# Performance work log

Hardware: AMD Instinct MI355X
Metric: run time of the kernel (lower is better)

Reference implementation:

```python
import jax, jax.numpy as jnp
import numpy as np

EMB_DIM = 768
HEAD_SIZE = 64


def setup_inputs() -> dict:
    key = jax.random.key(0)
    kx, kk, kq, kv = jax.random.split(key, 4)
    B, S = 8, 2048
    bound = 1.0 / np.sqrt(EMB_DIM)  # torch Linear default init range
    x = jax.random.normal(kx, (B, S, EMB_DIM), dtype=jnp.float32)
    Wk = jax.random.uniform(kk, (EMB_DIM, HEAD_SIZE), jnp.float32, -bound, bound)
    Wq = jax.random.uniform(kq, (EMB_DIM, HEAD_SIZE), jnp.float32, -bound, bound)
    Wv = jax.random.uniform(kv, (EMB_DIM, HEAD_SIZE), jnp.float32, -bound, bound)
    return {"x": x, "Wk": Wk, "Wq": Wq, "Wv": Wv}


def reference(x, Wk, Wq, Wv):
    # bias-free projections: [b, s, d] @ [d, h] -> [b, s, h]
    key = jnp.einsum("bsd,dh->bsh", x, Wk)
    query = jnp.einsum("bsd,dh->bsh", x, Wq)
    value = jnp.einsum("bsd,dh->bsh", x, Wv)
    scale = 1.0 / jnp.sqrt(jnp.asarray(HEAD_SIZE, dtype=x.dtype))
    # [b, q, k] attention scores
    scores = jnp.einsum("bqh,bkh->bqk", query, key) * scale
    probs = jax.nn.softmax(scores, axis=-1)
    # weighted value sum: [b, q, h]
    out = jnp.einsum("bqk,bkh->bqh", probs, value)
    return out
```

## Files before the change

### kernel.cpp

```cpp
#include <hip/hip_runtime.h>
#include <hip/hip_bf16.h>
#include <stdint.h>

#define B_ 8
#define S_ 2048
#define D_ 768
#define H_ 64
#define M_ (B_*S_)

typedef __attribute__((ext_vector_type(8))) short bf16x8;
typedef __attribute__((ext_vector_type(4))) float f32x4;
typedef __attribute__((ext_vector_type(4))) float floatv4;
typedef __attribute__((ext_vector_type(4))) unsigned short u16x4;
typedef __attribute__((ext_vector_type(8))) unsigned short u16x8;

__device__ __forceinline__ uint16_t f2bf(float f) {
    union { float f; uint32_t u; } c; c.f = f;
    return (uint16_t)((c.u + 0x7FFFu + ((c.u >> 16) & 1u)) >> 16);
}

__device__ __forceinline__ void load_lds16(const void* g, void* l) {
    __builtin_amdgcn_global_load_lds(
        (const __attribute__((address_space(1))) uint32_t*)(const uint32_t*)g,
        (__attribute__((address_space(3))) uint32_t*)(uint32_t*)l,
        16, 0, 0);
}

__global__ __launch_bounds__(256) void k_convert_w(const float* __restrict__ Wk,
                                                   const float* __restrict__ Wq,
                                                   const float* __restrict__ Wv,
                                                   uint16_t* __restrict__ wt) {
    const int mat = blockIdx.y;
    const float* W = mat == 0 ? Wk : (mat == 1 ? Wq : Wv);
    const float scale = (mat == 1) ? 0.18033688011f : 1.0f;
    uint16_t* out = wt + (size_t)mat * (H_ * D_);
    int i = blockIdx.x * 256 + threadIdx.x;
    int d = i >> 6, h = i & 63;
    out[h * D_ + d] = f2bf(W[i] * scale);
}

__global__ __launch_bounds__(512, 2) void k_proj(const float* __restrict__ x,
                                                 const uint16_t* __restrict__ wt,
                                                 uint16_t* __restrict__ kb,
                                                 uint16_t* __restrict__ qb,
                                                 uint16_t* __restrict__ vt) {
    __shared__ char lds[65536];
    const int tid  = threadIdx.x;
    const int lane = tid & 63, wave = tid >> 6;
    const int l15  = lane & 15, g = lane >> 4;
    const int m0   = blockIdx.x * 64;
    const int mrow = (wave >> 1) * 16;
    const int nb   = (wave & 1) * 32;

    const int trow = tid >> 3, tc8 = tid & 7;
    const float* xrowp = x + (size_t)(m0 + trow) * D_ + tc8 * 8;
    const int xw = trow * 128 + ((tc8 ^ (trow & 7)) << 4);

    const int cswz = (((lane & 7) ^ (lane >> 3)) << 4);
    const char* wsrc[3];
    int wdst[3];
#pragma unroll
    for (int j = 0; j < 3; ++j) {
        int c = wave * 3 + j, mat = c >> 3, wrow = (c & 7) * 8 + (lane >> 3);
        wsrc[j] = (const char*)(wt + (size_t)mat * (H_ * D_) + (size_t)wrow * D_) + cswz;
        wdst[j] = 16384 + c * 1024;
    }

    floatv4 xr[12][2];
#pragma unroll
    for (int kt = 0; kt < 12; ++kt) {
        xr[kt][0] = *(const floatv4*)(xrowp + kt * 64);
        xr[kt][1] = *(const floatv4*)(xrowp + kt * 64 + 4);
    }

#pragma unroll
    for (int j = 0; j < 3; ++j)
        load_lds16(wsrc[j], lds + wdst[j]);
    {
        u16x8 cv;
        cv[0]=f2bf(xr[0][0][0]); cv[1]=f2bf(xr[0][0][1]); cv[2]=f2bf(xr[0][0][2]); cv[3]=f2bf(xr[0][0][3]);
        cv[4]=f2bf(xr[0][1][0]); cv[5]=f2bf(xr[0][1][1]); cv[6]=f2bf(xr[0][1][2]); cv[7]=f2bf(xr[0][1][3]);
        *(u16x8*)(lds + xw) = cv;
    }
    __syncthreads();

    f32x4 acc[3][2] = {};

#pragma unroll
    for (int kt = 0; kt < 12; ++kt) {
        const int cur = kt & 1, nxt = cur ^ 1;
        if (kt < 11) {
#pragma unroll
            for (int j = 0; j < 3; ++j)
                load_lds16(wsrc[j] + (size_t)(kt + 1) * 128, lds + nxt * 24576 + wdst[j]);
        }
        const char* xsb = lds + cur * 8192;
        const char* wsb = lds + 16384 + cur * 24576;
        bf16x8 a[2], b[3][2][2];
#pragma unroll
        for (int kk = 0; kk < 2; ++kk) {
            int row = mrow + l15;
            a[kk] = *(const bf16x8*)(xsb + row * 128 + ((kk*64 + g*16) ^ ((row & 7) << 4)));
        }
#pragma unroll
        for (int mat = 0; mat < 3; ++mat)
#pragma unroll
            for (int n = 0; n < 2; ++n)
#pragma unroll
                for (int kk = 0; kk < 2; ++kk) {
                    int row = nb + n * 16 + l15;
                    b[mat][n][kk] = *(const bf16x8*)(wsb + mat * 8192 + row * 128 +
                                                     ((kk*64 + g*16) ^ ((row & 7) << 4)));
                }
#pragma unroll
        for (int mat = 0; mat < 3; ++mat)
#pragma unroll
            for (int n = 0; n < 2; ++n)
#pragma unroll
                for (int kk = 0; kk < 2; ++kk)
                    acc[mat][n] = __builtin_amdgcn_mfma_f32_16x16x32_bf16(
                                      a[kk], b[mat][n][kk], acc[mat][n], 0, 0, 0);
        if (kt < 11) {
            u16x8 cv;
            cv[0]=f2bf(xr[kt+1][0][0]); cv[1]=f2bf(xr[kt+1][0][1]);
            cv[2]=f2bf(xr[kt+1][0][2]); cv[3]=f2bf(xr[kt+1][0][3]);
            cv[4]=f2bf(xr[kt+1][1][0]); cv[5]=f2bf(xr[kt+1][1][1]);
            cv[6]=f2bf(xr[kt+1][1][2]); cv[7]=f2bf(xr[kt+1][1][3]);
            *(u16x8*)(lds + nxt * 8192 + xw) = cv;
        }
        __syncthreads();
    }

#pragma unroll
    for (int mat = 0; mat < 3; ++mat)
#pragma unroll
        for (int n = 0; n < 2; ++n) {
            int col  = nb + n * 16 + l15;
            int row0 = m0 + mrow + g * 4;
            if (mat < 2) {
                uint16_t* out = (mat == 0) ? kb : qb;
#pragma unroll
                for (int r = 0; r < 4; ++r)
                    out[(size_t)(row0 + r) * H_ + col] = f2bf(acc[mat][n][r]);
            } else {
                int bb = row0 >> 11, s = row0 & 2047;
                u16x4 pk;
#pragma unroll
                for (int r = 0; r < 4; ++r) pk[r] = f2bf(acc[mat][n][r]);
                *(u16x4*)(vt + ((size_t)bb * H_ + col) * S_ + s) = pk;
            }
        }
}

__global__ __launch_bounds__(256) void k_attn(const uint16_t* __restrict__ qb,
                                              const uint16_t* __restrict__ kb,
                                              const uint16_t* __restrict__ vt,
                                              float* __restrict__ out) {
    __shared__ char plds[4][4096];
    __shared__ float o_buf[4 * 32 * 64];
    __shared__ float l_buf[4][32];
    const int tid  = threadIdx.x;
    const int lane = tid & 63, wave = tid >> 6;
    const int l15 = lane & 15, g = lane >> 4;
    const int batch = blockIdx.y;
    const int q0 = blockIdx.x * 32;
    const size_t qrow = (size_t)batch * S_ + q0;
    const float MBIAS = 4.0f;

    bf16x8 aq[2][2];
#pragma unroll
    for (int qm = 0; qm < 2; ++qm)
#pragma unroll
        for (int kk = 0; kk < 2; ++kk)
            aq[qm][kk] = *(const bf16x8*)(qb + (qrow + qm*16 + l15) * H_ + kk*32 + g*8);

    f32x4 o[2][4] = {};
    float Ls[2][4] = {};

    const uint16_t* kbase = kb + (size_t)batch * S_ * H_;
    const uint16_t* vbase = vt + (size_t)batch * H_ * S_;
    char* pl = plds[wave];
    const int kt0 = wave * 8;

    bf16x8 bk[4][2], bkn[4][2];
#pragma unroll
    for (int n = 0; n < 4; ++n)
#pragma unroll
        for (int kk = 0; kk < 2; ++kk)
            bk[n][kk] = *(const bf16x8*)(kbase + (size_t)(kt0*64 + n*16 + l15) * H_ + kk*32 + g*8);

#pragma unroll
    for (int j = 0; j < 8; ++j) {
        const int kt = kt0 + j;
        if (j < 7) {
#pragma unroll
            for (int n = 0; n < 4; ++n)
#pragma unroll
                for (int kk = 0; kk < 2; ++kk)
                    bkn[n][kk] = *(const bf16x8*)(kbase + (size_t)((kt+1)*64 + n*16 + l15) * H_ + kk*32 + g*8);
        }
        f32x4 s[2][4] = {};
#pragma unroll
        for (int qm = 0; qm < 2; ++qm)
#pragma unroll
            for (int n = 0; n < 4; ++n)
#pragma unroll
                for (int kk = 0; kk < 2; ++kk)
                    s[qm][n] = __builtin_amdgcn_mfma_f32_16x16x32_bf16(
                                   aq[qm][kk], bk[n][kk], s[qm][n], 0, 0, 0);

        bf16x8 bv[4][2];
#pragma unroll
        for (int nh = 0; nh < 4; ++nh)
#pragma unroll
            for (int kk = 0; kk < 2; ++kk)
                bv[nh][kk] = *(const bf16x8*)(vbase + (size_t)(nh*16 + l15) * S_ + kt*64 + kk*32 + g*8);

#pragma unroll
        for (int qm = 0; qm < 2; ++qm)
#pragma unroll
            for (int r = 0; r < 4; ++r) {
                int row = qm*16 + g*4 + r;
#pragma unroll
                for (int n = 0; n < 4; ++n) {
                    float p = exp2f(s[qm][n][r] - MBIAS);
                    Ls[qm][r] += p;
                    int cb  = ((n*16 + l15) * 2) ^ ((row & 7) << 4);
                    *(uint16_t*)(pl + row*128 + cb) = f2bf(p);
                }
            }

        bf16x8 pa[2][2];
#pragma unroll
        for (int qm = 0; qm < 2; ++qm)
#pragma unroll
            for (int kk = 0; kk < 2; ++kk) {
                int row = qm*16 + l15;
                int cb  = (kk*64 + g*16) ^ ((row & 7) << 4);
                pa[qm][kk] = *(const bf16x8*)(pl + row*128 + cb);
            }
#pragma unroll
        for (int qm = 0; qm < 2; ++qm)
#pragma unroll
            for (int nh = 0; nh < 4; ++nh)
#pragma unroll
                for (int kk = 0; kk < 2; ++kk)
                    o[qm][nh] = __builtin_amdgcn_mfma_f32_16x16x32_bf16(
                                    pa[qm][kk], bv[nh][kk], o[qm][nh], 0, 0, 0);
        if (j < 7) {
#pragma unroll
            for (int n = 0; n < 4; ++n)
#pragma unroll
                for (int kk = 0; kk < 2; ++kk)
                    bk[n][kk] = bkn[n][kk];
        }
    }

#pragma unroll
    for (int qm = 0; qm < 2; ++qm)
#pragma unroll
        for (int r = 0; r < 4; ++r) {
            float l = Ls[qm][r];
#pragma unroll
            for (int off = 1; off < 16; off <<= 1) l += __shfl_xor(l, off);
            Ls[qm][r] = l;
        }
    if (l15 == 0) {
#pragma unroll
        for (int qm = 0; qm < 2; ++qm)
#pragma unroll
            for (int r = 0; r < 4; ++r)
                l_buf[wave][qm*16 + g*4 + r] = Ls[qm][r];
    }
#pragma unroll
    for (int qm = 0; qm < 2; ++qm)
#pragma unroll
        for (int nh = 0; nh < 4; ++nh)
#pragma unroll
            for (int r = 0; r < 4; ++r) {
                int i = qm*16 + nh*4 + r;
                o_buf[(wave*32 + i)*64 + lane] = o[qm][nh][r];
            }
    __syncthreads();

    const int iw0 = wave * 8;
    const int qm0 = iw0 >> 4;
    float rinv[4];
#pragma unroll
    for (int r = 0; r < 4; ++r) {
        int row = qm0*16 + g*4 + r;
        rinv[r] = 1.0f / (l_buf[0][row] + l_buf[1][row] + l_buf[2][row] + l_buf[3][row]);
    }
    float* obase = out + qrow * H_;
#pragma unroll
    for (int ii = 0; ii < 8; ++ii) {
        int i = iw0 + ii;
        int nh = (i >> 2) & 3, r = i & 3;
        float tot = o_buf[(0*32 + i)*64 + lane] + o_buf[(1*32 + i)*64 + lane]
                  + o_buf[(2*32 + i)*64 + lane] + o_buf[(3*32 + i)*64 + lane];
        int row = qm0*16 + g*4 + r, col = nh*16 + l15;
        obase[(size_t)row * H_ + col] = tot * rinv[r];
    }
}

extern "C" void kernel_launch(void* const* d_in, const int* in_sizes, int n_in,
                              void* d_out, int out_size, void* d_ws, size_t ws_size,
                              hipStream_t stream) {
    const float* x  = (const float*)d_in[0];
    const float* Wk = (const float*)d_in[1];
    const float* Wq = (const float*)d_in[2];
    const float* Wv = (const float*)d_in[3];
    float* out = (float*)d_out;

    uint16_t* ws = (uint16_t*)d_ws;
    uint16_t* wt = ws;
    uint16_t* kb = wt + (size_t)3 * H_ * D_;
    uint16_t* qb = kb + (size_t)M_ * H_;
    uint16_t* vt = qb + (size_t)M_ * H_;

    k_convert_w<<<dim3(192, 3), dim3(256), 0, stream>>>(Wk, Wq, Wv, wt);
    k_proj<<<dim3(M_ / 64), dim3(512), 0, stream>>>(x, wt, kb, qb, vt);
    k_attn<<<dim3(S_ / 32, B_), dim3(256), 0, stream>>>(qb, kb, vt, out);
}
```

Baseline: 130.8 us.

## Halve projection tile rows and interleave two key tiles per attention iteration

The projection kernel now processes 32 rows per block instead of 64, with each wave computing one 16-column slice across the three matrices. This doubles the grid and cuts per-thread register and LDS use, at the cost of reloading the weights more often. The attention kernel now handles two independent key tiles per loop iteration with separate score, probability buffer and output accumulators, exposing more independent MFMA and memory work to hide latency. The cost is more register pressure and the loss of explicit next-tile K prefetch.

```diff
diff --git a/kernel.cpp b/kernel.cpp
--- a/kernel.cpp
+++ b/kernel.cpp
@@ -39,22 +39,22 @@
     out[h * D_ + d] = f2bf(W[i] * scale);
 }
 
-__global__ __launch_bounds__(512, 2) void k_proj(const float* __restrict__ x,
-                                                 const uint16_t* __restrict__ wt,
-                                                 uint16_t* __restrict__ kb,
-                                                 uint16_t* __restrict__ qb,
-                                                 uint16_t* __restrict__ vt) {
-    __shared__ char lds[65536];
+__global__ __launch_bounds__(512) void k_proj(const float* __restrict__ x,
+                                              const uint16_t* __restrict__ wt,
+                                              uint16_t* __restrict__ kb,
+                                              uint16_t* __restrict__ qb,
+                                              uint16_t* __restrict__ vt) {
+    __shared__ char lds[57344];
     const int tid  = threadIdx.x;
     const int lane = tid & 63, wave = tid >> 6;
     const int l15  = lane & 15, g = lane >> 4;
-    const int m0   = blockIdx.x * 64;
-    const int mrow = (wave >> 1) * 16;
-    const int nb   = (wave & 1) * 32;
-
-    const int trow = tid >> 3, tc8 = tid & 7;
-    const float* xrowp = x + (size_t)(m0 + trow) * D_ + tc8 * 8;
-    const int xw = trow * 128 + ((tc8 ^ (trow & 7)) << 4);
+    const int m0   = blockIdx.x * 32;
+    const int mrow = (wave & 1) * 16;
+    const int nc   = (wave >> 1) * 16;
+
+    const int trow = tid >> 4, tc = tid & 15;
+    const float* xrowp = x + (size_t)(m0 + trow) * D_ + tc * 4;
+    const int xw = trow * 128 + (((tc >> 1) ^ (trow & 7)) << 4) + (tc & 1) * 8;
 
     const int cswz = (((lane & 7) ^ (lane >> 3)) << 4);
     const char* wsrc[3];
@@ -63,28 +63,25 @@
     for (int j = 0; j < 3; ++j) {
         int c = wave * 3 + j, mat = c >> 3, wrow = (c & 7) * 8 + (lane >> 3);
         wsrc[j] = (const char*)(wt + (size_t)mat * (H_ * D_) + (size_t)wrow * D_) + cswz;
-        wdst[j] = 16384 + c * 1024;
-    }
-
-    floatv4 xr[12][2];
-#pragma unroll
-    for (int kt = 0; kt < 12; ++kt) {
-        xr[kt][0] = *(const floatv4*)(xrowp + kt * 64);
-        xr[kt][1] = *(const floatv4*)(xrowp + kt * 64 + 4);
-    }
+        wdst[j] = 8192 + c * 1024;
+    }
+
+    floatv4 xr[12];
+#pragma unroll
+    for (int kt = 0; kt < 12; ++kt)
+        xr[kt] = *(const floatv4*)(xrowp + kt * 64);
 
 #pragma unroll
     for (int j = 0; j < 3; ++j)
         load_lds16(wsrc[j], lds + wdst[j]);
     {
-        u16x8 cv;
-        cv[0]=f2bf(xr[0][0][0]); cv[1]=f2bf(xr[0][0][1]); cv[2]=f2bf(xr[0][0][2]); cv[3]=f2bf(xr[0][0][3]);
-        cv[4]=f2bf(xr[0][1][0]); cv[5]=f2bf(xr[0][1][1]); cv[6]=f2bf(xr[0][1][2]); cv[7]=f2bf(xr[0][1][3]);
-        *(u16x8*)(lds + xw) = cv;
+        u16x4 cv;
+        cv[0]=f2bf(xr[0][0]); cv[1]=f2bf(xr[0][1]); cv[2]=f2bf(xr[0][2]); cv[3]=f2bf(xr[0][3]);
+        *(u16x4*)(lds + xw) = cv;
     }
     __syncthreads();
 
-    f32x4 acc[3][2] = {};
+    f32x4 acc[3] = {};
 
 #pragma unroll
     for (int kt = 0; kt < 12; ++kt) {
@@ -94,9 +91,9 @@
             for (int j = 0; j < 3; ++j)
                 load_lds16(wsrc[j] + (size_t)(kt + 1) * 128, lds + nxt * 24576 + wdst[j]);
         }
-        const char* xsb = lds + cur * 8192;
-        const char* wsb = lds + 16384 + cur * 24576;
-        bf16x8 a[2], b[3][2][2];
+        const char* xsb = lds + cur * 4096;
+        const char* wsb = lds + 8192 + cur * 24576;
+        bf16x8 a[2], b[3][2];
 #pragma unroll
         for (int kk = 0; kk < 2; ++kk) {
             int row = mrow + l15;
@@ -105,60 +102,50 @@
 #pragma unroll
         for (int mat = 0; mat < 3; ++mat)
 #pragma unroll
-            for (int n = 0; n < 2; ++n)
-#pragma unroll
-                for (int kk = 0; kk < 2; ++kk) {
-                    int row = nb + n * 16 + l15;
-                    b[mat][n][kk] = *(const bf16x8*)(wsb + mat * 8192 + row * 128 +
-                                                     ((kk*64 + g*16) ^ ((row & 7) << 4)));
-                }
+            for (int kk = 0; kk < 2; ++kk) {
+                int row = nc + l15;
+                b[mat][kk] = *(const bf16x8*)(wsb + mat * 8192 + row * 128 +
+                                              ((kk*64 + g*16) ^ ((row & 7) << 4)));
+            }
 #pragma unroll
         for (int mat = 0; mat < 3; ++mat)
 #pragma unroll
-            for (int n = 0; n < 2; ++n)
-#pragma unroll
-                for (int kk = 0; kk < 2; ++kk)
-                    acc[mat][n] = __builtin_amdgcn_mfma_f32_16x16x32_bf16(
-                                      a[kk], b[mat][n][kk], acc[mat][n], 0, 0, 0);
+            for (int kk = 0; kk < 2; ++kk)
+                acc[mat] = __builtin_amdgcn_mfma_f32_16x16x32_bf16(
+                               a[kk], b[mat][kk], acc[mat], 0, 0, 0);
         if (kt < 11) {
-            u16x8 cv;
-            cv[0]=f2bf(xr[kt+1][0][0]); cv[1]=f2bf(xr[kt+1][0][1]);
-            cv[2]=f2bf(xr[kt+1][0][2]); cv[3]=f2bf(xr[kt+1][0][3]);
-            cv[4]=f2bf(xr[kt+1][1][0]); cv[5]=f2bf(xr[kt+1][1][1]);
-            cv[6]=f2bf(xr[kt+1][1][2]); cv[7]=f2bf(xr[kt+1][1][3]);
-            *(u16x8*)(lds + nxt * 8192 + xw) = cv;
+            u16x4 cv;
+            cv[0]=f2bf(xr[kt+1][0]); cv[1]=f2bf(xr[kt+1][1]);
+            cv[2]=f2bf(xr[kt+1][2]); cv[3]=f2bf(xr[kt+1][3]);
+            *(u16x4*)(lds + nxt * 4096 + xw) = cv;
         }
         __syncthreads();
     }
 
 #pragma unroll
-    for (int mat = 0; mat < 3; ++mat)
-#pragma unroll
-        for (int n = 0; n < 2; ++n) {
-            int col  = nb + n * 16 + l15;
-            int row0 = m0 + mrow + g * 4;
-            if (mat < 2) {
-                uint16_t* out = (mat == 0) ? kb : qb;
-#pragma unroll
-                for (int r = 0; r < 4; ++r)
-                    out[(size_t)(row0 + r) * H_ + col] = f2bf(acc[mat][n][r]);
-            } else {
-                int bb = row0 >> 11, s = row0 & 2047;
-                u16x4 pk;
-#pragma unroll
-                for (int r = 0; r < 4; ++r) pk[r] = f2bf(acc[mat][n][r]);
-                *(u16x4*)(vt + ((size_t)bb * H_ + col) * S_ + s) = pk;
-            }
-        }
+    for (int mat = 0; mat < 3; ++mat) {
+        int col  = nc + l15;
+        int row0 = m0 + mrow + g * 4;
+        if (mat < 2) {
+            uint16_t* out = (mat == 0) ? kb : qb;
+#pragma unroll
+            for (int r = 0; r < 4; ++r)
+                out[(size_t)(row0 + r) * H_ + col] = f2bf(acc[mat][r]);
+        } else {
+            int bb = row0 >> 11, s = row0 & 2047;
+            u16x4 pk;
+#pragma unroll
+            for (int r = 0; r < 4; ++r) pk[r] = f2bf(acc[mat][r]);
+            *(u16x4*)(vt + ((size_t)bb * H_ + col) * S_ + s) = pk;
+        }
+    }
 }
 
 __global__ __launch_bounds__(256) void k_attn(const uint16_t* __restrict__ qb,
                                               const uint16_t* __restrict__ kb,
                                               const uint16_t* __restrict__ vt,
                                               float* __restrict__ out) {
-    __shared__ char plds[4][4096];
-    __shared__ float o_buf[4 * 32 * 64];
-    __shared__ float l_buf[4][32];
+    __shared__ char smem[65536];
     const int tid  = threadIdx.x;
     const int lane = tid & 63, wave = tid >> 6;
     const int l15 = lane & 15, g = lane >> 4;
@@ -167,6 +154,8 @@
     const size_t qrow = (size_t)batch * S_ + q0;
     const float MBIAS = 4.0f;
 
+    float* o_buf = (float*)(smem + 32768);
+
     bf16x8 aq[2][2];
 #pragma unroll
     for (int qm = 0; qm < 2; ++qm)
@@ -174,47 +163,66 @@
         for (int kk = 0; kk < 2; ++kk)
             aq[qm][kk] = *(const bf16x8*)(qb + (qrow + qm*16 + l15) * H_ + kk*32 + g*8);
 
-    f32x4 o[2][4] = {};
-    float Ls[2][4] = {};
+    f32x4 o[2][2][4] = {};
+    float Ls[2][2][4] = {};
 
     const uint16_t* kbase = kb + (size_t)batch * S_ * H_;
     const uint16_t* vbase = vt + (size_t)batch * H_ * S_;
-    char* pl = plds[wave];
+    char* pl0 = smem + wave * 8192;
+    char* pl1 = pl0 + 4096;
     const int kt0 = wave * 8;
 
-    bf16x8 bk[4][2], bkn[4][2];
-#pragma unroll
-    for (int n = 0; n < 4; ++n)
-#pragma unroll
-        for (int kk = 0; kk < 2; ++kk)
-            bk[n][kk] = *(const bf16x8*)(kbase + (size_t)(kt0*64 + n*16 + l15) * H_ + kk*32 + g*8);
-
-#pragma unroll
-    for (int j = 0; j < 8; ++j) {
-        const int kt = kt0 + j;
-        if (j < 7) {
+#pragma unroll
+    for (int i = 0; i < 4; ++i) {
+        const int ktA = kt0 + i, ktB = kt0 + 4 + i;
+
+        f32x4 sA[2][4] = {};
+        bf16x8 bvA[4][2];
+        {
+            bf16x8 bk[4][2];
 #pragma unroll
             for (int n = 0; n < 4; ++n)
 #pragma unroll
                 for (int kk = 0; kk < 2; ++kk)
-                    bkn[n][kk] = *(const bf16x8*)(kbase + (size_t)((kt+1)*64 + n*16 + l15) * H_ + kk*32 + g*8);
-        }
-        f32x4 s[2][4] = {};
-#pragma unroll
-        for (int qm = 0; qm < 2; ++qm)
+                    bk[n][kk] = *(const bf16x8*)(kbase + (size_t)(ktA*64 + n*16 + l15) * H_ + kk*32 + g*8);
+#pragma unroll
+            for (int qm = 0; qm < 2; ++qm)
+#pragma unroll
+                for (int n = 0; n < 4; ++n)
+#pragma unroll
+                    for (int kk = 0; kk < 2; ++kk)
+                        sA[qm][n] = __builtin_amdgcn_mfma_f32_16x16x32_bf16(
+                                        aq[qm][kk], bk[n][kk], sA[qm][n], 0, 0, 0);
+#pragma unroll
+            for (int nh = 0; nh < 4; ++nh)
+#pragma unroll
+                for (int kk = 0; kk < 2; ++kk)
+                    bvA[nh][kk] = *(const bf16x8*)(vbase + (size_t)(nh*16 + l15) * S_ + ktA*64 + kk*32 + g*8);
+        }
+
+        f32x4 sB[2][4] = {};
+        bf16x8 bvB[4][2];
+        {
+            bf16x8 bk[4][2];
 #pragma unroll
             for (int n = 0; n < 4; ++n)
 #pragma unroll
                 for (int kk = 0; kk < 2; ++kk)
-                    s[qm][n] = __builtin_amdgcn_mfma_f32_16x16x32_bf16(
-                                   aq[qm][kk], bk[n][kk], s[qm][n], 0, 0, 0);
-
-        bf16x8 bv[4][2];
-#pragma unroll
-        for (int nh = 0; nh < 4; ++nh)
-#pragma unroll
-            for (int kk = 0; kk < 2; ++kk)
-                bv[nh][kk] = *(const bf16x8*)(vbase + (size_t)(nh*16 + l15) * S_ + kt*64 + kk*32 + g*8);
+                    bk[n][kk] = *(const bf16x8*)(kbase + (size_t)(ktB*64 + n*16 + l15) * H_ + kk*32 + g*8);
+#pragma unroll
+            for (int qm = 0; qm < 2; ++qm)
+#pragma unroll
+                for (int n = 0; n < 4; ++n)
+#pragma unroll
+                    for (int kk = 0; kk < 2; ++kk)
+                        sB[qm][n] = __builtin_amdgcn_mfma_f32_16x16x32_bf16(
+                                        aq[qm][kk], bk[n][kk], sB[qm][n], 0, 0, 0);
+#pragma unroll
+            for (int nh = 0; nh < 4; ++nh)
+#pragma unroll
+                for (int kk = 0; kk < 2; ++kk)
+                    bvB[nh][kk] = *(const bf16x8*)(vbase + (size_t)(nh*16 + l15) * S_ + ktB*64 + kk*32 + g*8);
+        }
 
 #pragma unroll
         for (int qm = 0; qm < 2; ++qm)
@@ -223,55 +231,57 @@
                 int row = qm*16 + g*4 + r;
 #pragma unroll
                 for (int n = 0; n < 4; ++n) {
-                    float p = exp2f(s[qm][n][r] - MBIAS);
-                    Ls[qm][r] += p;
-                    int cb  = ((n*16 + l15) * 2) ^ ((row & 7) << 4);
-                    *(uint16_t*)(pl + row*128 + cb) = f2bf(p);
+                    int cb = ((n*16 + l15) * 2) ^ ((row & 7) << 4);
+                    float pA = exp2f(sA[qm][n][r] - MBIAS);
+                    Ls[0][qm][r] += pA;
+                    *(uint16_t*)(pl0 + row*128 + cb) = f2bf(pA);
+                    float pB = exp2f(sB[qm][n][r] - MBIAS);
+                    Ls[1][qm][r] += pB;
+                    *(uint16_t*)(pl1 + row*128 + cb) = f2bf(pB);
                 }
             }
 
-        bf16x8 pa[2][2];
+        bf16x8 paA[2][2], paB[2][2];
 #pragma unroll
         for (int qm = 0; qm < 2; ++qm)
 #pragma unroll
             for (int kk = 0; kk < 2; ++kk) {
                 int row = qm*16 + l15;
                 int cb  = (kk*64 + g*16) ^ ((row & 7) << 4);
-                pa[qm][kk] = *(const bf16x8*)(pl + row*128 + cb);
+                paA[qm][kk] = *(const bf16x8*)(pl0 + row*128 + cb);
+                paB[qm][kk] = *(const bf16x8*)(pl1 + row*128 + cb);
             }
 #pragma unroll
         for (int qm = 0; qm < 2; ++qm)
 #pragma unroll
             for (int nh = 0; nh < 4; ++nh)
 #pragma unroll
-                for (int kk = 0; kk < 2; ++kk)
-                    o[qm][nh] = __builtin_amdgcn_mfma_f32_16x16x32_bf16(
-                                    pa[qm][kk], bv[nh][kk], o[qm][nh], 0, 0, 0);
-        if (j < 7) {
-#pragma unroll
-            for (int n = 0; n < 4; ++n)
-#pragma unroll
-                for (int kk = 0; kk < 2; ++kk)
-                    bk[n][kk] = bkn[n][kk];
-        }
-    }
-
+                for (int kk = 0; kk < 2; ++kk) {
+                    o[0][qm][nh] = __builtin_amdgcn_mfma_f32_16x16x32_bf16(
+                                       paA[qm][kk], bvA[nh][kk], o[0][qm][nh], 0, 0, 0);
+                    o[1][qm][nh] = __builtin_amdgcn_mfma_f32_16x16x32_bf16(
+                                       paB[qm][kk], bvB[nh][kk], o[1][qm][nh], 0, 0, 0);
+                }
+    }
+
+#pragma unroll
+    for (int qm = 0; qm < 2; ++qm) {
+#pragma unroll
+        for (int nh = 0; nh < 4; ++nh) o[0][qm][nh] += o[1][qm][nh];
+#pragma unroll
+        for (int r = 0; r < 4; ++r) Ls[0][qm][r] += Ls[1][qm][r];
+    }
+
+    float* l_buf = (float*)(smem + wave * 8192);
 #pragma unroll
     for (int qm = 0; qm < 2; ++qm)
 #pragma unroll
         for (int r = 0; r < 4; ++r) {
-            float l = Ls[qm][r];
+            float l = Ls[0][qm][r];
 #pragma unroll
             for (int off = 1; off < 16; off <<= 1) l += __shfl_xor(l, off);
-            Ls[qm][r] = l;
-        }
-    if (l15 == 0) {
-#pragma unroll
-        for (int qm = 0; qm < 2; ++qm)
-#pragma unroll
-            for (int r = 0; r < 4; ++r)
-                l_buf[wave][qm*16 + g*4 + r] = Ls[qm][r];
-    }
+            if (l15 == 0) l_buf[qm*16 + g*4 + r] = l;
+        }
 #pragma unroll
     for (int qm = 0; qm < 2; ++qm)
 #pragma unroll
@@ -279,7 +289,7 @@
 #pragma unroll
             for (int r = 0; r < 4; ++r) {
                 int i = qm*16 + nh*4 + r;
-                o_buf[(wave*32 + i)*64 + lane] = o[qm][nh][r];
+                o_buf[(wave*32 + i)*64 + lane] = o[0][qm][nh][r];
             }
     __syncthreads();
 
@@ -289,7 +299,11 @@
 #pragma unroll
     for (int r = 0; r < 4; ++r) {
         int row = qm0*16 + g*4 + r;
-        rinv[r] = 1.0f / (l_buf[0][row] + l_buf[1][row] + l_buf[2][row] + l_buf[3][row]);
+        float lt = 0.f;
+#pragma unroll
+        for (int wv = 0; wv < 4; ++wv)
+            lt += *(float*)(smem + wv*8192 + (row)*4);
+        rinv[r] = 1.0f / lt;
     }
     float* obase = out + qrow * H_;
 #pragma unroll
@@ -319,6 +333,6 @@
     uint16_t* vt = qb + (size_t)M_ * H_;
 
     k_convert_w<<<dim3(192, 3), dim3(256), 0, stream>>>(Wk, Wq, Wv, wt);
-    k_proj<<<dim3(M_ / 64), dim3(512), 0, stream>>>(x, wt, kb, qb, vt);
+    k_proj<<<dim3(M_ / 32), dim3(512), 0, stream>>>(x, wt, kb, qb, vt);
     k_attn<<<dim3(S_ / 32, B_), dim3(256), 0, stream>>>(qb, kb, vt, out);
 }
```

Measured after the change: 144.3 us. 10.4% more time.
